# Kernel optimization log

Hardware: AMD Instinct MI355X
Metric: run time of the kernel (lower is better)

Reference implementation:

```python
import jax, jax.numpy as jnp
import numpy as np

D_MODEL = 256
N_HEADS = 8
D_HEAD = D_MODEL // N_HEADS
B = 65536
LN_EPS = 1e-5


def setup_inputs() -> dict:
    key = jax.random.key(0)
    ks = jax.random.split(key, 6)
    s = 1.0 / np.sqrt(D_MODEL)
    x = jax.random.normal(ks[0], (B, D_MODEL), dtype=jnp.float32)
    Wq = jax.random.normal(ks[1], (D_MODEL, D_MODEL), dtype=jnp.float32) * s
    Wk = jax.random.normal(ks[2], (D_MODEL, D_MODEL), dtype=jnp.float32) * s
    Wv = jax.random.normal(ks[3], (D_MODEL, D_MODEL), dtype=jnp.float32) * s
    Wout = jax.random.normal(ks[4], (D_MODEL, D_MODEL), dtype=jnp.float32) * s
    b_out = jnp.zeros((D_MODEL,), dtype=jnp.float32)
    # L initialized to identity per head (matches nn.init.eye_) plus tiny noise
    L = jnp.broadcast_to(jnp.eye(D_HEAD, dtype=jnp.float32), (N_HEADS, D_HEAD, D_HEAD)) \
        + 0.01 * jax.random.normal(ks[5], (N_HEADS, D_HEAD, D_HEAD), dtype=jnp.float32)
    gamma = jnp.ones((D_MODEL,), dtype=jnp.float32)
    beta = jnp.zeros((D_MODEL,), dtype=jnp.float32)
    return {"x": x, "Wq": Wq, "Wk": Wk, "Wv": Wv, "Wout": Wout,
            "b_out": b_out, "L": L, "gamma": gamma, "beta": beta}


def reference(x, Wq, Wk, Wv, Wout, b_out, L, gamma, beta):
    b = x.shape[0]
    # projections; view as [B, H, d_head]
    Q = (x @ Wq).reshape(b, N_HEADS, D_HEAD)
    K = (x @ Wk).reshape(b, N_HEADS, D_HEAD)
    V = (x @ Wv).reshape(b, N_HEADS, D_HEAD)
    # pairwise head differences: [B, Hq, Hk, d_head]
    diff = Q[:, :, None, :] - K[:, None, :, :]
    # per-key-head learned metric transform: L indexed by key head
    diff_t = jnp.einsum('bqkd,kdf->bqkf', diff, L)
    sq_dist = jnp.sum(diff_t * diff_t, axis=-1)            # [B, Hq, Hk]
    attn = jax.nn.softmax(-sq_dist / jnp.sqrt(jnp.float32(D_HEAD)), axis=2)
    out = jnp.einsum('bqk,bkd->bqd', attn, V).reshape(b, D_MODEL)
    out = out @ Wout + b_out
    h = out + x
    # LayerNorm over last dim
    mu = jnp.mean(h, axis=-1, keepdims=True)
    var = jnp.mean((h - mu) ** 2, axis=-1, keepdims=True)
    return (h - mu) * jax.lax.rsqrt(var + LN_EPS) * gamma + beta
```

## Files before the change

kernel.cpp:

```cpp
#include <hip/hip_runtime.h>


typedef __bf16 bf16x8 __attribute__((ext_vector_type(8)));
typedef float  f32x4  __attribute__((ext_vector_type(4)));
typedef int    i32x4  __attribute__((ext_vector_type(4)));
typedef int    i32x2  __attribute__((ext_vector_type(2)));
typedef unsigned short u16;

__device__ __forceinline__ float bf2f(u16 u){
  unsigned int x = ((unsigned int)u) << 16;
  return __builtin_bit_cast(float, x);
}
__device__ __forceinline__ u16 f2bf(float f){
  unsigned int u = __builtin_bit_cast(unsigned int, f);
  u += 0x7FFFu + ((u >> 16) & 1u);
  return (u16)(u >> 16);
}
__device__ __forceinline__ unsigned int pk2(float lo, float hi){
  return ((unsigned int)f2bf(hi) << 16) | (unsigned int)f2bf(lo);
}
__device__ __forceinline__ bf16x8 ldfrag_lds(const u16* p){
  return __builtin_bit_cast(bf16x8, *(const i32x4*)p);
}
__device__ __forceinline__ bf16x8 ldfrag_g(const u16* p){
  return __builtin_bit_cast(bf16x8, *(const i32x4*)p);
}

#define LROW 264

__global__ __launch_bounds__(256) void geo_prep(
    const float* __restrict__ Wq, const float* __restrict__ Wk,
    const float* __restrict__ Wv, const float* __restrict__ Wout,
    const float* __restrict__ L, u16* __restrict__ ws)
{
  const int b = blockIdx.x, t = threadIdx.x;
  if (b < 64){
    const int m = b >> 4;
    const float* src = (m == 0) ? Wq : (m == 1) ? Wk : (m == 2) ? Wv : Wout;
    u16* dstbase = (m < 3) ? (ws + m*65536) : (ws + 196608);
    const int tile = b & 15;
    const int tr = tile >> 2, tc = tile & 3;
    __shared__ float tlf[64][68];
    {
      const int row = t >> 2, cs = (t & 3)*16;
      #pragma unroll
      for (int j = 0; j < 4; ++j){
        f32x4 v = *(const f32x4*)(src + (size_t)(tr*64 + row)*256 + tc*64 + cs + j*4);
        #pragma unroll
        for (int p = 0; p < 4; ++p) tlf[row][cs + j*4 + p] = v[p];
      }
    }
    __syncthreads();
    {
      const int n = t >> 2, cs = (t & 3)*16;
      float us[16];
      #pragma unroll
      for (int j = 0; j < 16; ++j) us[j] = tlf[cs + j][n];
      #pragma unroll
      for (int h = 0; h < 2; ++h){
        i32x4 o;
        #pragma unroll
        for (int p = 0; p < 4; ++p)
          o[p] = (int)pk2(us[h*8 + 2*p], us[h*8 + 2*p + 1]);
        *(i32x4*)(dstbase + (size_t)(tc*64 + n)*256 + tr*64 + cs + h*8) = o;
      }
    }
  } else {
    u16* Lt = ws + 262144;
    const int k = t >> 5, f = t & 31;
    for (int d = 0; d < 32; ++d)
      Lt[k*1024 + f*32 + d] = f2bf(L[k*1024 + d*32 + f]);
  }
}

__global__ __launch_bounds__(512, 4) void geo_fused(
    const float* __restrict__ x,     const u16* __restrict__ WqkvT,
    const u16* __restrict__ WoutT,   const u16* __restrict__ Lt,
    const float* __restrict__ b_out, const float* __restrict__ gamma,
    const float* __restrict__ beta,  float* __restrict__ out)
{
  __shared__ __align__(16) char pool[67584];
  u16* xsU  = (u16*)(pool);
  u16* KtsU = (u16*)(pool);
  u16* QsU  = (u16*)(pool + 16896);
  u16* hsU  = (u16*)(pool + 16896);
  u16* KsU  = (u16*)(pool + 33792);
  u16* aoU  = (u16*)(pool + 33792);
  u16* VsU  = (u16*)(pool + 50688);

  const int t    = threadIdx.x;
  const int lane = t & 63;
  const int w    = t >> 6;
  const int l15  = lane & 15;
  const int quad = lane >> 4;
  const long rowbase = (long)blockIdx.x * 32;

  {
    const int r  = t >> 4;
    const int c0 = (t & 15) * 16;
    const float* src = x + (rowbase + r)*256 + c0;
    unsigned int wds[8];
    #pragma unroll
    for (int j = 0; j < 4; ++j){
      f32x4 v = *(const f32x4*)(src + j*4);
      wds[j*2    ] = pk2(v[0], v[1]);
      wds[j*2 + 1] = pk2(v[2], v[3]);
    }
    #pragma unroll
    for (int h = 0; h < 2; ++h){
      i32x4 o;
      #pragma unroll
      for (int p = 0; p < 4; ++p) o[p] = (int)wds[h*4 + p];
      *(i32x4*)&xsU[r*LROW + c0 + h*8] = o;
    }
  }
  __syncthreads();

  #pragma unroll
  for (int s = 0; s < 3; ++s){
    const u16* Bbase = WqkvT + (size_t)(s*256 + w*32)*256;
    u16* dst = (s == 0) ? QsU : (s == 1) ? KsU : VsU;
    f32x4 acc[2][2];
    #pragma unroll
    for (int mt = 0; mt < 2; ++mt)
      #pragma unroll
      for (int nt = 0; nt < 2; ++nt) acc[mt][nt] = f32x4{0.f,0.f,0.f,0.f};
    #pragma unroll
    for (int kk = 0; kk < 8; ++kk){
      const int c0 = kk*32 + quad*8;
      bf16x8 a[2], bb[2];
      #pragma unroll
      for (int mt = 0; mt < 2; ++mt) a[mt] = ldfrag_lds(&xsU[(mt*16 + l15)*LROW + c0]);
      #pragma unroll
      for (int nt = 0; nt < 2; ++nt) bb[nt] = ldfrag_g(Bbase + (size_t)(nt*16 + l15)*256 + c0);
      #pragma unroll
      for (int mt = 0; mt < 2; ++mt)
        #pragma unroll
        for (int nt = 0; nt < 2; ++nt)
          acc[mt][nt] = __builtin_amdgcn_mfma_f32_16x16x32_bf16(a[mt], bb[nt], acc[mt][nt], 0, 0, 0);
    }
    #pragma unroll
    for (int mt = 0; mt < 2; ++mt)
      #pragma unroll
      for (int nt = 0; nt < 2; ++nt){
        const int col = w*32 + nt*16 + l15;
        #pragma unroll
        for (int reg = 0; reg < 4; ++reg)
          dst[(mt*16 + quad*4 + reg)*LROW + col] = f2bf(acc[mt][nt][reg]);
      }
  }
  __syncthreads();

  {
    bf16x8 aL[2], bK[2];
    #pragma unroll
    for (int mt = 0; mt < 2; ++mt)
      aL[mt] = ldfrag_g(Lt + w*1024 + (mt*16 + l15)*32 + quad*8);
    #pragma unroll
    for (int nt = 0; nt < 2; ++nt)
      bK[nt] = ldfrag_lds(&KsU[(nt*16 + l15)*LROW + w*32 + quad*8]);
    f32x4 acc[2][2];
    #pragma unroll
    for (int mt = 0; mt < 2; ++mt)
      #pragma unroll
      for (int nt = 0; nt < 2; ++nt)
        acc[mt][nt] = __builtin_amdgcn_mfma_f32_16x16x32_bf16(aL[mt], bK[nt],
                        f32x4{0.f,0.f,0.f,0.f}, 0, 0, 0);
    #pragma unroll
    for (int mt = 0; mt < 2; ++mt)
      #pragma unroll
      for (int nt = 0; nt < 2; ++nt){
        i32x2 o;
        o[0] = (int)pk2(acc[mt][nt][0], acc[mt][nt][1]);
        o[1] = (int)pk2(acc[mt][nt][2], acc[mt][nt][3]);
        *(i32x2*)&KtsU[w*1024 + (nt*16 + l15)*32 + mt*16 + quad*4] = o;
      }
  }
  __syncthreads();

  float lg[2][8];
  {
    bf16x8 bQ[2];
    #pragma unroll
    for (int nt = 0; nt < 2; ++nt)
      bQ[nt] = ldfrag_lds(&QsU[(nt*16 + l15)*LROW + w*32 + quad*8]);
    #pragma unroll
    for (int k = 0; k < 8; ++k){
      bf16x8 aL[2];
      #pragma unroll
      for (int mt = 0; mt < 2; ++mt)
        aL[mt] = ldfrag_g(Lt + k*1024 + (mt*16 + l15)*32 + quad*8);
      f32x4 acc[2][2];
      #pragma unroll
      for (int mt = 0; mt < 2; ++mt)
        #pragma unroll
        for (int nt = 0; nt < 2; ++nt)
          acc[mt][nt] = __builtin_amdgcn_mfma_f32_16x16x32_bf16(aL[mt], bQ[nt],
                          f32x4{0.f,0.f,0.f,0.f}, 0, 0, 0);
      #pragma unroll
      for (int nt = 0; nt < 2; ++nt){
        float s = 0.f;
        #pragma unroll
        for (int mt = 0; mt < 2; ++mt){
          i32x2 kt2 = *(const i32x2*)&KtsU[k*1024 + (nt*16 + l15)*32 + mt*16 + quad*4];
          unsigned int u0 = (unsigned int)kt2[0], u1 = (unsigned int)kt2[1];
          float kv0 = __builtin_bit_cast(float, u0 << 16);
          float kv1 = __builtin_bit_cast(float, u0 & 0xFFFF0000u);
          float kv2 = __builtin_bit_cast(float, u1 << 16);
          float kv3 = __builtin_bit_cast(float, u1 & 0xFFFF0000u);
          float d0 = acc[mt][nt][0] - kv0, d1 = acc[mt][nt][1] - kv1;
          float d2 = acc[mt][nt][2] - kv2, d3 = acc[mt][nt][3] - kv3;
          s = fmaf(d0, d0, s); s = fmaf(d1, d1, s);
          s = fmaf(d2, d2, s); s = fmaf(d3, d3, s);
        }
        s += __shfl_xor(s, 16);
        s += __shfl_xor(s, 32);
        lg[nt][k] = s * -0.17677669529663687f;
      }
    }
  }
  __syncthreads();

  {
    #pragma unroll
    for (int nt = 0; nt < 2; ++nt){
      const int r = nt*16 + l15;
      float mx = lg[nt][0];
      #pragma unroll
      for (int k = 1; k < 8; ++k) mx = fmaxf(mx, lg[nt][k]);
      float e[8], sum = 0.f;
      #pragma unroll
      for (int k = 0; k < 8; ++k){ e[k] = __expf(lg[nt][k] - mx); sum += e[k]; }
      const float inv = 1.0f / sum;
      float o[8] = {0.f,0.f,0.f,0.f,0.f,0.f,0.f,0.f};
      #pragma unroll
      for (int k = 0; k < 8; ++k){
        i32x4 v = *(const i32x4*)&VsU[r*LROW + k*32 + quad*8];
        const float a = e[k] * inv;
        #pragma unroll
        for (int p = 0; p < 4; ++p){
          unsigned int u = (unsigned int)v[p];
          o[2*p    ] = fmaf(a, __builtin_bit_cast(float, u << 16),         o[2*p    ]);
          o[2*p + 1] = fmaf(a, __builtin_bit_cast(float, u & 0xFFFF0000u), o[2*p + 1]);
        }
      }
      i32x4 pkv;
      #pragma unroll
      for (int p = 0; p < 4; ++p) pkv[p] = (int)pk2(o[2*p], o[2*p + 1]);
      *(i32x4*)&aoU[r*LROW + w*32 + quad*8] = pkv;
    }
  }
  __syncthreads();

  {
    f32x4 acc[2][2];
    #pragma unroll
    for (int mt = 0; mt < 2; ++mt)
      #pragma unroll
      for (int nt = 0; nt < 2; ++nt) acc[mt][nt] = f32x4{0.f,0.f,0.f,0.f};
    #pragma unroll
    for (int kk = 0; kk < 8; ++kk){
      const int c0 = kk*32 + quad*8;
      bf16x8 a[2], bb[2];
      #pragma unroll
      for (int mt = 0; mt < 2; ++mt) a[mt] = ldfrag_lds(&aoU[(mt*16 + l15)*LROW + c0]);
      #pragma unroll
      for (int nt = 0; nt < 2; ++nt)
        bb[nt] = ldfrag_g(WoutT + (size_t)(w*32 + nt*16 + l15)*256 + c0);
      #pragma unroll
      for (int mt = 0; mt < 2; ++mt)
        #pragma unroll
        for (int nt = 0; nt < 2; ++nt)
          acc[mt][nt] = __builtin_amdgcn_mfma_f32_16x16x32_bf16(a[mt], bb[nt], acc[mt][nt], 0, 0, 0);
    }
    #pragma unroll
    for (int nt = 0; nt < 2; ++nt){
      const int col = w*32 + nt*16 + l15;
      const float bo = b_out[col];
      #pragma unroll
      for (int mt = 0; mt < 2; ++mt)
        #pragma unroll
        for (int reg = 0; reg < 4; ++reg)
          hsU[(mt*16 + quad*4 + reg)*256 + col] = f2bf(acc[mt][nt][reg] + bo);
    }
  }
  __syncthreads();

  {
    #pragma unroll
    for (int rr = 0; rr < 4; ++rr){
      const int r = w*4 + rr;
      const int c = lane*4;
      i32x2 h2 = *(const i32x2*)&hsU[r*256 + c];
      f32x4 xv = *(const f32x4*)(x + (rowbase + r)*256 + c);
      unsigned int u0 = (unsigned int)h2[0], u1 = (unsigned int)h2[1];
      f32x4 hv;
      hv[0] = __builtin_bit_cast(float, u0 << 16)         + xv[0];
      hv[1] = __builtin_bit_cast(float, u0 & 0xFFFF0000u) + xv[1];
      hv[2] = __builtin_bit_cast(float, u1 << 16)         + xv[2];
      hv[3] = __builtin_bit_cast(float, u1 & 0xFFFF0000u) + xv[3];
      float s  = hv[0] + hv[1] + hv[2] + hv[3];
      float s2 = hv[0]*hv[0] + hv[1]*hv[1] + hv[2]*hv[2] + hv[3]*hv[3];
      #pragma unroll
      for (int off = 1; off < 64; off <<= 1){
        s  += __shfl_xor(s,  off);
        s2 += __shfl_xor(s2, off);
      }
      const float mu  = s  * (1.0f/256.0f);
      const float var = s2 * (1.0f/256.0f) - mu*mu;
      const float rs  = rsqrtf(var + 1e-5f);
      f32x4 gv = *(const f32x4*)(gamma + c);
      f32x4 bv = *(const f32x4*)(beta  + c);
      f32x4 y;
      y[0] = (hv[0] - mu)*rs*gv[0] + bv[0];
      y[1] = (hv[1] - mu)*rs*gv[1] + bv[1];
      y[2] = (hv[2] - mu)*rs*gv[2] + bv[2];
      y[3] = (hv[3] - mu)*rs*gv[3] + bv[3];
      *(f32x4*)(out + (rowbase + r)*256 + c) = y;
    }
  }
}

extern "C" void kernel_launch(void* const* d_in, const int* in_sizes, int n_in,
                              void* d_out, int out_size, void* d_ws, size_t ws_size,
                              hipStream_t stream)
{
  const float* x     = (const float*)d_in[0];
  const float* Wq    = (const float*)d_in[1];
  const float* Wk    = (const float*)d_in[2];
  const float* Wv    = (const float*)d_in[3];
  const float* Wout  = (const float*)d_in[4];
  const float* b_out = (const float*)d_in[5];
  const float* L     = (const float*)d_in[6];
  const float* gamma = (const float*)d_in[7];
  const float* beta  = (const float*)d_in[8];
  u16* ws = (u16*)d_ws;

  geo_prep<<<65, 256, 0, stream>>>(Wq, Wk, Wv, Wout, L, ws);
  geo_fused<<<2048, 512, 0, stream>>>(x, ws, ws + 196608, ws + 262144,
                                      b_out, gamma, beta, (float*)d_out);
}
```

Before: 265.0 us.

## Fold L into Wk, compute K' directly into registers and shrink LDS

The prep kernel now premultiplies Wk by the per-head metric L, so the fused kernel computes L-transformed keys with one GEMM into registers instead of projecting K to LDS and running an extra MFMA stage. Dropping the K buffer shrinks LDS per block, which lets the launch bound target 6 blocks per CU instead of 4. The transformed K is stored with an XOR-swizzled layout to reduce bank conflicts, and hs gets a padded row stride. The trade-offs are extra register pressure from holding the K accumulators across the Q/V stage, and a change in rounding because L is folded into the bf16-rounded weight.

```diff
diff --git a/kernel.cpp b/kernel.cpp
--- a/kernel.cpp
+++ b/kernel.cpp
@@ -27,6 +27,10 @@
 }
 
 #define LROW 264
+
+__device__ __forceinline__ int kts_off(int k, int r, int fb){
+  return (k*2048 + r*64 + fb*2) ^ ((r & 7) << 4);
+}
 
 __global__ __launch_bounds__(256) void geo_prep(
     const float* __restrict__ Wq, const float* __restrict__ Wk,
@@ -54,8 +58,22 @@
     {
       const int n = t >> 2, cs = (t & 3)*16;
       float us[16];
-      #pragma unroll
-      for (int j = 0; j < 16; ++j) us[j] = tlf[cs + j][n];
+      if (m == 1){
+        const int hh = n >> 5, f = n & 31;
+        const int kg = tc*2 + hh;
+        #pragma unroll
+        for (int j = 0; j < 16; ++j) us[j] = 0.f;
+        #pragma unroll 4
+        for (int d = 0; d < 32; ++d){
+          const float lv = L[kg*1024 + d*32 + f];
+          #pragma unroll
+          for (int j = 0; j < 16; ++j)
+            us[j] = fmaf(tlf[cs + j][hh*32 + d], lv, us[j]);
+        }
+      } else {
+        #pragma unroll
+        for (int j = 0; j < 16; ++j) us[j] = tlf[cs + j][n];
+      }
       #pragma unroll
       for (int h = 0; h < 2; ++h){
         i32x4 o;
@@ -73,20 +91,19 @@
   }
 }
 
-__global__ __launch_bounds__(512, 4) void geo_fused(
+__global__ __launch_bounds__(512, 6) void geo_fused(
     const float* __restrict__ x,     const u16* __restrict__ WqkvT,
     const u16* __restrict__ WoutT,   const u16* __restrict__ Lt,
     const float* __restrict__ b_out, const float* __restrict__ gamma,
     const float* __restrict__ beta,  float* __restrict__ out)
 {
-  __shared__ __align__(16) char pool[67584];
-  u16* xsU  = (u16*)(pool);
-  u16* KtsU = (u16*)(pool);
-  u16* QsU  = (u16*)(pool + 16896);
-  u16* hsU  = (u16*)(pool + 16896);
-  u16* KsU  = (u16*)(pool + 33792);
-  u16* aoU  = (u16*)(pool + 33792);
-  u16* VsU  = (u16*)(pool + 50688);
+  __shared__ __align__(16) char pool[50688];
+  u16*  xsU  = (u16*)(pool);
+  char* ktsB = pool;
+  u16*  hsU  = (u16*)(pool);
+  u16*  QsU  = (u16*)(pool + 16896);
+  u16*  aoU  = (u16*)(pool + 16896);
+  u16*  VsU  = (u16*)(pool + 33792);
 
   const int t    = threadIdx.x;
   const int lane = t & 63;
@@ -117,9 +134,10 @@
   __syncthreads();
 
   #pragma unroll
-  for (int s = 0; s < 3; ++s){
+  for (int si = 0; si < 2; ++si){
+    const int s = si << 1;
     const u16* Bbase = WqkvT + (size_t)(s*256 + w*32)*256;
-    u16* dst = (s == 0) ? QsU : (s == 1) ? KsU : VsU;
+    u16* dst = si ? VsU : QsU;
     f32x4 acc[2][2];
     #pragma unroll
     for (int mt = 0; mt < 2; ++mt)
@@ -149,31 +167,41 @@
           dst[(mt*16 + quad*4 + reg)*LROW + col] = f2bf(acc[mt][nt][reg]);
       }
   }
-  __syncthreads();
-
-  {
-    bf16x8 aL[2], bK[2];
-    #pragma unroll
-    for (int mt = 0; mt < 2; ++mt)
-      aL[mt] = ldfrag_g(Lt + w*1024 + (mt*16 + l15)*32 + quad*8);
-    #pragma unroll
-    for (int nt = 0; nt < 2; ++nt)
-      bK[nt] = ldfrag_lds(&KsU[(nt*16 + l15)*LROW + w*32 + quad*8]);
-    f32x4 acc[2][2];
-    #pragma unroll
-    for (int mt = 0; mt < 2; ++mt)
-      #pragma unroll
-      for (int nt = 0; nt < 2; ++nt)
-        acc[mt][nt] = __builtin_amdgcn_mfma_f32_16x16x32_bf16(aL[mt], bK[nt],
-                        f32x4{0.f,0.f,0.f,0.f}, 0, 0, 0);
+
+  f32x4 kacc[2][2];
+  {
+    #pragma unroll
+    for (int mt = 0; mt < 2; ++mt)
+      #pragma unroll
+      for (int nt = 0; nt < 2; ++nt) kacc[mt][nt] = f32x4{0.f,0.f,0.f,0.f};
+    const u16* Abase = WqkvT + (size_t)(256 + w*32)*256;
+    #pragma unroll
+    for (int kk = 0; kk < 8; ++kk){
+      const int c0 = kk*32 + quad*8;
+      bf16x8 aW[2], bX[2];
+      #pragma unroll
+      for (int mt = 0; mt < 2; ++mt) aW[mt] = ldfrag_g(Abase + (size_t)(mt*16 + l15)*256 + c0);
+      #pragma unroll
+      for (int nt = 0; nt < 2; ++nt) bX[nt] = ldfrag_lds(&xsU[(nt*16 + l15)*LROW + c0]);
+      #pragma unroll
+      for (int mt = 0; mt < 2; ++mt)
+        #pragma unroll
+        for (int nt = 0; nt < 2; ++nt)
+          kacc[mt][nt] = __builtin_amdgcn_mfma_f32_16x16x32_bf16(aW[mt], bX[nt], kacc[mt][nt], 0, 0, 0);
+    }
+  }
+  __syncthreads();
+
+  {
     #pragma unroll
     for (int mt = 0; mt < 2; ++mt)
       #pragma unroll
       for (int nt = 0; nt < 2; ++nt){
+        const int r = nt*16 + l15;
         i32x2 o;
-        o[0] = (int)pk2(acc[mt][nt][0], acc[mt][nt][1]);
-        o[1] = (int)pk2(acc[mt][nt][2], acc[mt][nt][3]);
-        *(i32x2*)&KtsU[w*1024 + (nt*16 + l15)*32 + mt*16 + quad*4] = o;
+        o[0] = (int)pk2(kacc[mt][nt][0], kacc[mt][nt][1]);
+        o[1] = (int)pk2(kacc[mt][nt][2], kacc[mt][nt][3]);
+        *(i32x2*)(ktsB + kts_off(w, r, mt*16 + quad*4)) = o;
       }
   }
   __syncthreads();
@@ -199,10 +227,11 @@
                           f32x4{0.f,0.f,0.f,0.f}, 0, 0, 0);
       #pragma unroll
       for (int nt = 0; nt < 2; ++nt){
+        const int r = nt*16 + l15;
         float s = 0.f;
         #pragma unroll
         for (int mt = 0; mt < 2; ++mt){
-          i32x2 kt2 = *(const i32x2*)&KtsU[k*1024 + (nt*16 + l15)*32 + mt*16 + quad*4];
+          i32x2 kt2 = *(const i32x2*)(ktsB + kts_off(k, r, mt*16 + quad*4));
           unsigned int u0 = (unsigned int)kt2[0], u1 = (unsigned int)kt2[1];
           float kv0 = __builtin_bit_cast(float, u0 << 16);
           float kv1 = __builtin_bit_cast(float, u0 & 0xFFFF0000u);
@@ -281,7 +310,7 @@
       for (int mt = 0; mt < 2; ++mt)
         #pragma unroll
         for (int reg = 0; reg < 4; ++reg)
-          hsU[(mt*16 + quad*4 + reg)*256 + col] = f2bf(acc[mt][nt][reg] + bo);
+          hsU[(mt*16 + quad*4 + reg)*LROW + col] = f2bf(acc[mt][nt][reg] + bo);
     }
   }
   __syncthreads();
@@ -291,7 +320,7 @@
     for (int rr = 0; rr < 4; ++rr){
       const int r = w*4 + rr;
       const int c = lane*4;
-      i32x2 h2 = *(const i32x2*)&hsU[r*256 + c];
+      i32x2 h2 = *(const i32x2*)&hsU[r*LROW + c];
       f32x4 xv = *(const f32x4*)(x + (rowbase + r)*256 + c);
       unsigned int u0 = (unsigned int)h2[0], u1 = (unsigned int)h2[1];
       f32x4 hv;
```

After: 261.9 us. Within noise of the previous version (-1.2%).

## Fold Q-K difference and metric L into precomputed per-head-pair weights

Applied to the files above, without the earlier changes.

Precomputes, for each query/key head pair, a combined weight (Wq_head - Wk_head)·L_k in the prep kernel, so diff_t is computed directly as x times that weight. This removes the separate Q and K projections, the L transforms of Q and K, and their LDS buffers, which shrinks shared memory and lets the launch bound request more blocks per CU. In exchange the fused kernel runs 8x more MFMA work for the distance stage (a 256-wide K loop per head pair instead of a 32-wide one) and streams a 1 MB bf16 weight array from global/L2.

```diff
diff --git a/kernel.cpp b/kernel.cpp
--- a/kernel.cpp
+++ b/kernel.cpp
@@ -7,10 +7,6 @@
 typedef int    i32x2  __attribute__((ext_vector_type(2)));
 typedef unsigned short u16;
 
-__device__ __forceinline__ float bf2f(u16 u){
-  unsigned int x = ((unsigned int)u) << 16;
-  return __builtin_bit_cast(float, x);
-}
 __device__ __forceinline__ u16 f2bf(float f){
   unsigned int u = __builtin_bit_cast(unsigned int, f);
   u += 0x7FFFu + ((u >> 16) & 1u);
@@ -35,10 +31,36 @@
 {
   const int b = blockIdx.x, t = threadIdx.x;
   if (b < 64){
-    const int m = b >> 4;
-    const float* src = (m == 0) ? Wq : (m == 1) ? Wk : (m == 2) ? Wv : Wout;
-    u16* dstbase = (m < 3) ? (ws + m*65536) : (ws + 196608);
-    const int tile = b & 15;
+    const int w = b >> 3, k = b & 7;
+    __shared__ float Lsh[32][33];
+    #pragma unroll
+    for (int i = 0; i < 4; ++i){
+      const int idx = t*4 + i;
+      Lsh[idx >> 5][idx & 31] = L[k*1024 + idx];
+    }
+    __syncthreads();
+    float diffv[32];
+    #pragma unroll
+    for (int j4 = 0; j4 < 8; ++j4){
+      f32x4 qv = *(const f32x4*)(Wq + (size_t)t*256 + w*32 + j4*4);
+      f32x4 kv = *(const f32x4*)(Wk + (size_t)t*256 + k*32 + j4*4);
+      #pragma unroll
+      for (int p = 0; p < 4; ++p) diffv[j4*4 + p] = qv[p] - kv[p];
+    }
+    u16* dst = ws + (size_t)w*65536 + (size_t)(k*32)*256 + t;
+    #pragma unroll 4
+    for (int f = 0; f < 32; ++f){
+      float s = 0.f;
+      #pragma unroll
+      for (int j = 0; j < 32; ++j) s = fmaf(diffv[j], Lsh[j][f], s);
+      dst[(size_t)f*256] = f2bf(s);
+    }
+  } else {
+    const int bb = b - 64;
+    const int mm = bb >> 4;
+    const float* src = mm ? Wout : Wv;
+    u16* dstbase = ws + 524288 + mm*65536;
+    const int tile = bb & 15;
     const int tr = tile >> 2, tc = tile & 3;
     __shared__ float tlf[64][68];
     {
@@ -65,28 +87,20 @@
         *(i32x4*)(dstbase + (size_t)(tc*64 + n)*256 + tr*64 + cs + h*8) = o;
       }
     }
-  } else {
-    u16* Lt = ws + 262144;
-    const int k = t >> 5, f = t & 31;
-    for (int d = 0; d < 32; ++d)
-      Lt[k*1024 + f*32 + d] = f2bf(L[k*1024 + d*32 + f]);
-  }
-}
-
-__global__ __launch_bounds__(512, 4) void geo_fused(
-    const float* __restrict__ x,     const u16* __restrict__ WqkvT,
-    const u16* __restrict__ WoutT,   const u16* __restrict__ Lt,
+  }
+}
+
+__global__ __launch_bounds__(512, 6) void geo_fused(
+    const float* __restrict__ x,     const u16* __restrict__ WdT,
+    const u16* __restrict__ WvT,     const u16* __restrict__ WoutT,
     const float* __restrict__ b_out, const float* __restrict__ gamma,
     const float* __restrict__ beta,  float* __restrict__ out)
 {
-  __shared__ __align__(16) char pool[67584];
-  u16* xsU  = (u16*)(pool);
-  u16* KtsU = (u16*)(pool);
-  u16* QsU  = (u16*)(pool + 16896);
-  u16* hsU  = (u16*)(pool + 16896);
-  u16* KsU  = (u16*)(pool + 33792);
-  u16* aoU  = (u16*)(pool + 33792);
-  u16* VsU  = (u16*)(pool + 50688);
+  __shared__ __align__(16) char pool[33792];
+  u16* xsU = (u16*)(pool);
+  u16* aoU = (u16*)(pool);
+  u16* VsU = (u16*)(pool + 16896);
+  u16* hsU = (u16*)(pool + 16896);
 
   const int t    = threadIdx.x;
   const int lane = t & 63;
@@ -116,10 +130,7 @@
   }
   __syncthreads();
 
-  #pragma unroll
-  for (int s = 0; s < 3; ++s){
-    const u16* Bbase = WqkvT + (size_t)(s*256 + w*32)*256;
-    u16* dst = (s == 0) ? QsU : (s == 1) ? KsU : VsU;
+  {
     f32x4 acc[2][2];
     #pragma unroll
     for (int mt = 0; mt < 2; ++mt)
@@ -132,7 +143,8 @@
       #pragma unroll
       for (int mt = 0; mt < 2; ++mt) a[mt] = ldfrag_lds(&xsU[(mt*16 + l15)*LROW + c0]);
       #pragma unroll
-      for (int nt = 0; nt < 2; ++nt) bb[nt] = ldfrag_g(Bbase + (size_t)(nt*16 + l15)*256 + c0);
+      for (int nt = 0; nt < 2; ++nt)
+        bb[nt] = ldfrag_g(WvT + (size_t)(w*32 + nt*16 + l15)*256 + c0);
       #pragma unroll
       for (int mt = 0; mt < 2; ++mt)
         #pragma unroll
@@ -146,73 +158,45 @@
         const int col = w*32 + nt*16 + l15;
         #pragma unroll
         for (int reg = 0; reg < 4; ++reg)
-          dst[(mt*16 + quad*4 + reg)*LROW + col] = f2bf(acc[mt][nt][reg]);
-      }
-  }
-  __syncthreads();
-
-  {
-    bf16x8 aL[2], bK[2];
-    #pragma unroll
-    for (int mt = 0; mt < 2; ++mt)
-      aL[mt] = ldfrag_g(Lt + w*1024 + (mt*16 + l15)*32 + quad*8);
-    #pragma unroll
-    for (int nt = 0; nt < 2; ++nt)
-      bK[nt] = ldfrag_lds(&KsU[(nt*16 + l15)*LROW + w*32 + quad*8]);
-    f32x4 acc[2][2];
-    #pragma unroll
-    for (int mt = 0; mt < 2; ++mt)
-      #pragma unroll
-      for (int nt = 0; nt < 2; ++nt)
-        acc[mt][nt] = __builtin_amdgcn_mfma_f32_16x16x32_bf16(aL[mt], bK[nt],
-                        f32x4{0.f,0.f,0.f,0.f}, 0, 0, 0);
-    #pragma unroll
-    for (int mt = 0; mt < 2; ++mt)
-      #pragma unroll
-      for (int nt = 0; nt < 2; ++nt){
-        i32x2 o;
-        o[0] = (int)pk2(acc[mt][nt][0], acc[mt][nt][1]);
-        o[1] = (int)pk2(acc[mt][nt][2], acc[mt][nt][3]);
-        *(i32x2*)&KtsU[w*1024 + (nt*16 + l15)*32 + mt*16 + quad*4] = o;
-      }
-  }
-  __syncthreads();
+          VsU[(mt*16 + quad*4 + reg)*LROW + col] = f2bf(acc[mt][nt][reg]);
+      }
+  }
 
   float lg[2][8];
   {
-    bf16x8 bQ[2];
-    #pragma unroll
-    for (int nt = 0; nt < 2; ++nt)
-      bQ[nt] = ldfrag_lds(&QsU[(nt*16 + l15)*LROW + w*32 + quad*8]);
+    const u16* Wd_w = WdT + (size_t)w*65536;
     #pragma unroll
     for (int k = 0; k < 8; ++k){
-      bf16x8 aL[2];
-      #pragma unroll
-      for (int mt = 0; mt < 2; ++mt)
-        aL[mt] = ldfrag_g(Lt + k*1024 + (mt*16 + l15)*32 + quad*8);
+      const u16* Ab = Wd_w + (size_t)(k*32)*256;
       f32x4 acc[2][2];
       #pragma unroll
-      for (int mt = 0; mt < 2; ++mt)
+      for (int ct = 0; ct < 2; ++ct)
+        #pragma unroll
+        for (int nt = 0; nt < 2; ++nt) acc[ct][nt] = f32x4{0.f,0.f,0.f,0.f};
+      #pragma unroll
+      for (int kk = 0; kk < 8; ++kk){
+        const int c0 = kk*32 + quad*8;
+        bf16x8 aW[2], bX[2];
+        #pragma unroll
+        for (int ct = 0; ct < 2; ++ct)
+          aW[ct] = ldfrag_g(Ab + (size_t)(ct*16 + l15)*256 + c0);
         #pragma unroll
         for (int nt = 0; nt < 2; ++nt)
-          acc[mt][nt] = __builtin_amdgcn_mfma_f32_16x16x32_bf16(aL[mt], bQ[nt],
-                          f32x4{0.f,0.f,0.f,0.f}, 0, 0, 0);
+          bX[nt] = ldfrag_lds(&xsU[(nt*16 + l15)*LROW + c0]);
+        #pragma unroll
+        for (int ct = 0; ct < 2; ++ct)
+          #pragma unroll
+          for (int nt = 0; nt < 2; ++nt)
+            acc[ct][nt] = __builtin_amdgcn_mfma_f32_16x16x32_bf16(aW[ct], bX[nt], acc[ct][nt], 0, 0, 0);
+      }
       #pragma unroll
       for (int nt = 0; nt < 2; ++nt){
         float s = 0.f;
         #pragma unroll
-        for (int mt = 0; mt < 2; ++mt){
-          i32x2 kt2 = *(const i32x2*)&KtsU[k*1024 + (nt*16 + l15)*32 + mt*16 + quad*4];
-          unsigned int u0 = (unsigned int)kt2[0], u1 = (unsigned int)kt2[1];
-          float kv0 = __builtin_bit_cast(float, u0 << 16);
-          float kv1 = __builtin_bit_cast(float, u0 & 0xFFFF0000u);
-          float kv2 = __builtin_bit_cast(float, u1 << 16);
-          float kv3 = __builtin_bit_cast(float, u1 & 0xFFFF0000u);
-          float d0 = acc[mt][nt][0] - kv0, d1 = acc[mt][nt][1] - kv1;
-          float d2 = acc[mt][nt][2] - kv2, d3 = acc[mt][nt][3] - kv3;
-          s = fmaf(d0, d0, s); s = fmaf(d1, d1, s);
-          s = fmaf(d2, d2, s); s = fmaf(d3, d3, s);
-        }
+        for (int ct = 0; ct < 2; ++ct)
+          #pragma unroll
+          for (int reg = 0; reg < 4; ++reg)
+            s = fmaf(acc[ct][nt][reg], acc[ct][nt][reg], s);
         s += __shfl_xor(s, 16);
         s += __shfl_xor(s, 32);
         lg[nt][k] = s * -0.17677669529663687f;
@@ -336,7 +320,7 @@
   const float* beta  = (const float*)d_in[8];
   u16* ws = (u16*)d_ws;
 
-  geo_prep<<<65, 256, 0, stream>>>(Wq, Wk, Wv, Wout, L, ws);
-  geo_fused<<<2048, 512, 0, stream>>>(x, ws, ws + 196608, ws + 262144,
+  geo_prep<<<96, 256, 0, stream>>>(Wq, Wk, Wv, Wout, L, ws);
+  geo_fused<<<2048, 512, 0, stream>>>(x, ws, ws + 524288, ws + 589824,
                                       b_out, gamma, beta, (float*)d_out);
 }
```

After: 635.2 us. +139.7%, slower.
